# Kernel tuning notes

Measured on AMD Instinct MI355X. Metric: run time of the kernel, lower is better.

The kernel has to match this reference:

```python
import jax, jax.numpy as jnp
import numpy as np

# Cap on neighbors per query. The original op returns ragged (data-dependent
# length) neighbor lists, which is impossible under jit; we return a padded
# [M, K] representation plus row_splits built from the true (capped) counts.
K = 64


def setup_inputs() -> dict:
    key = jax.random.key(0)
    kp, kq = jax.random.split(key)
    points = jax.random.normal(kp, (16384, 3), dtype=jnp.float32)
    queries = jax.random.normal(kq, (8192, 3), dtype=jnp.float32)
    radius = jnp.asarray(0.15, dtype=jnp.float32)
    return {"points": points, "queries": queries, "radius": radius}


def _pairwise_sqdist(queries, points):
    # ||q-p||^2 = ||q||^2 + ||p||^2 - 2 q.p  (avoids an [M,N,3] intermediate)
    q2 = jnp.sum(queries * queries, axis=-1)  # [M]
    p2 = jnp.sum(points * points, axis=-1)    # [N]
    d2 = q2[:, None] + p2[None, :] - 2.0 * (queries @ points.T)  # [M,N]
    return jnp.maximum(d2, 0.0)


def reference(points, queries, radius):
    # metric='L2' -> squared distances, ignore_query_point=False,
    # return_distances=True.
    d2 = _pairwise_sqdist(queries, points)          # [M, N]
    mask = d2 <= radius * radius                    # neighbor membership
    # Select up to K closest in-radius neighbors per query via top_k on -d2.
    neg = jnp.where(mask, -d2, -jnp.inf)
    vals, idx = jax.lax.top_k(neg, K)               # [M, K]
    valid = vals > -jnp.inf                         # which slots hold real neighbors
    counts = jnp.sum(valid.astype(jnp.int64), axis=-1)          # [M]
    neighbors_row_splits = jnp.concatenate(
        [jnp.zeros((1,), jnp.int64), jnp.cumsum(counts)])       # [M+1]
    neighbors_index = jnp.where(valid, idx, -1)                 # [M, K], -1 pad
    neighbors_distance = jnp.where(valid, -vals, 0.0)           # [M, K], squared L2
    return neighbors_index, neighbors_row_splits, neighbors_distance
```

## Files before the change

### kernel.cpp

```cpp
#include <hip/hip_runtime.h>
#include <math.h>

#pragma clang fp contract(off)

#define KCAP 64
#define QPW 4
#define WAVES 4
#define BLOCK (WAVES * 64)
#define QPB (QPW * WAVES)
#define SLABS 4
#define TILE 1024

__global__ __launch_bounds__(256) void prep_kernel(
    const float* __restrict__ pts, float4* __restrict__ soa,
    int* __restrict__ counts, int N, int M) {
  int i = blockIdx.x * 256 + threadIdx.x;
  if (i < N) {
    float x = pts[i * 3 + 0];
    float y = pts[i * 3 + 1];
    float z = pts[i * 3 + 2];
    soa[i] = make_float4(x, y, z, (x * x + y * y) + z * z);
  }
  if (i < M) counts[i] = 0;
}

__global__ __launch_bounds__(BLOCK, 8) void search_kernel(
    const float4* __restrict__ soa, const float* __restrict__ queries,
    const float* __restrict__ radius_p, float* __restrict__ out_idx,
    float* __restrict__ out_dist, int* __restrict__ counts, int N, int M) {
  __shared__ float4 tile[TILE];
  const int tid = threadIdx.x;
  const int lane = tid & 63;
  const int wave = tid >> 6;
  const float r = radius_p[0];
  const float rr = r * r;
  const int qbase = (blockIdx.x * WAVES + wave) * QPW;
  const int slab = N / SLABS;
  const int slab_begin = blockIdx.y * slab;
  const int slab_end = slab_begin + slab;

  float qx[QPW], qy[QPW], qz[QPW], q2[QPW];
#pragma unroll
  for (int g = 0; g < QPW; ++g) {
    int q = qbase + g;
    float x = queries[q * 3 + 0];
    float y = queries[q * 3 + 1];
    float z = queries[q * 3 + 2];
    qx[g] = x; qy[g] = y; qz[g] = z;
    q2[g] = (x * x + y * y) + z * z;
  }

  for (int base = slab_begin; base < slab_end; base += TILE) {
    for (int i = tid; i < TILE; i += BLOCK) tile[i] = soa[base + i];
    __syncthreads();
#pragma unroll 4
    for (int it = 0; it < TILE / 64; ++it) {
      int j = it * 64 + lane;
      float4 p = tile[j];
      float d2v[QPW];
      bool hit[QPW];
      bool any = false;
#pragma unroll
      for (int g = 0; g < QPW; ++g) {
        float dot = fmaf(p.z, qz[g], fmaf(p.y, qy[g], p.x * qx[g]));
        float s = q2[g] + p.w;
        float d2 = fmaf(dot, -2.0f, s);
        d2 = fmaxf(d2, 0.0f);
        d2v[g] = d2;
        hit[g] = (d2 <= rr);
        any = any | hit[g];
      }
      if (any) {
#pragma unroll
        for (int g = 0; g < QPW; ++g)
          if (hit[g]) {
            int q = qbase + g;
            int pos = atomicAdd(&counts[q], 1);
            if (pos < KCAP) {
              out_dist[q * KCAP + pos] = d2v[g];
              out_idx[q * KCAP + pos] = (float)(base + j);
            }
          }
      }
    }
    __syncthreads();
  }
}

__global__ __launch_bounds__(256) void sort_kernel(
    float* __restrict__ out_idx, float* __restrict__ out_dist,
    int* __restrict__ counts, int M) {
  int q = blockIdx.x * (256 / 64) + (threadIdx.x >> 6);
  if (q >= M) return;
  int lane = threadIdx.x & 63;
  int c = counts[q];
  int c64 = c < KCAP ? c : KCAP;
  float d2 = (lane < c64) ? out_dist[q * KCAP + lane] : INFINITY;
  int idx = (lane < c64) ? (int)out_idx[q * KCAP + lane] : 0x7fffffff;
  for (int k = 2; k <= 64; k <<= 1) {
    for (int jj = k >> 1; jj > 0; jj >>= 1) {
      float od2 = __shfl_xor(d2, jj);
      int oidx = __shfl_xor(idx, jj);
      bool up = ((lane & k) == 0);
      bool lower = ((lane & jj) == 0);
      bool takeMin = (lower == up);
      bool oLess = (od2 < d2) || (od2 == d2 && oidx < idx);
      bool take = takeMin ? oLess : !oLess;
      if (take) { d2 = od2; idx = oidx; }
    }
  }
  out_idx[q * KCAP + lane] = (lane < c64) ? (float)idx : -1.0f;
  out_dist[q * KCAP + lane] = (lane < c64) ? d2 : 0.0f;
  if (lane == 0 && c != c64) counts[q] = c64;
}

__global__ __launch_bounds__(1024) void scan_kernel(
    const int* __restrict__ counts, float* __restrict__ rs, int M) {
  __shared__ int part[1024];
  const int tid = threadIdx.x;
  const int base = tid * 8;
  int loc[8];
  int s = 0;
  for (int j = 0; j < 8; ++j) {
    int c = (base + j < M) ? counts[base + j] : 0;
    c = c < KCAP ? c : KCAP;
    s += c;
    loc[j] = s;
  }
  part[tid] = s;
  __syncthreads();
  for (int off = 1; off < 1024; off <<= 1) {
    int v = (tid >= off) ? part[tid - off] : 0;
    __syncthreads();
    part[tid] += v;
    __syncthreads();
  }
  int excl = part[tid] - s;
  if (tid == 0) rs[0] = 0.0f;
  for (int j = 0; j < 8; ++j)
    if (base + j < M) rs[1 + base + j] = (float)(excl + loc[j]);
}

extern "C" void kernel_launch(void* const* d_in, const int* in_sizes, int n_in,
                              void* d_out, int out_size, void* d_ws, size_t ws_size,
                              hipStream_t stream) {
  const float* points = (const float*)d_in[0];
  const float* queries = (const float*)d_in[1];
  const float* radius = (const float*)d_in[2];
  const int N = in_sizes[0] / 3;
  const int M = in_sizes[1] / 3;

  float* out = (float*)d_out;
  float* out_idx = out;
  float* out_rs = out + (size_t)M * KCAP;
  float* out_dist = out_rs + (M + 1);

  float4* soa = (float4*)d_ws;
  int* counts = (int*)(soa + N);

  int prep_n = (N > M ? N : M);
  prep_kernel<<<(prep_n + 255) / 256, 256, 0, stream>>>(points, soa, counts, N, M);

  dim3 grid((M + QPB - 1) / QPB, SLABS);
  search_kernel<<<grid, BLOCK, 0, stream>>>(soa, queries, radius, out_idx,
                                            out_dist, counts, N, M);

  sort_kernel<<<(M + 3) / 4, 256, 0, stream>>>(out_idx, out_dist, counts, M);
  scan_kernel<<<1, 1024, 0, stream>>>(counts, out_rs, M);
}
```

Measured before the change: 52.57 us.

## Fuse prep into search, merge sort and scan, double queries per wave

Removes the prep kernel: the search kernel now loads AoS points directly into the shared tile and computes the squared norm there, and the counts are zeroed with a memset. Queries per wave go from 4 to 8 and slabs from 4 to 8, which gives more point reuse per tile load and more blocks, at the cost of more registers (launch bounds occupancy lowered to 6). The clamp to zero moves off the hot path into the rare hit branch. The sort and scan kernels are merged into a single finalize launch whose last block performs a wave-shuffle scan, cutting one launch.

New measurement: 67.69 us. 28.8% more time.

```diff
diff --git a/kernel.cpp b/kernel.cpp
--- a/kernel.cpp
+++ b/kernel.cpp
@@ -4,28 +4,15 @@
 #pragma clang fp contract(off)
 
 #define KCAP 64
-#define QPW 4
+#define QPW 8
 #define WAVES 4
 #define BLOCK (WAVES * 64)
 #define QPB (QPW * WAVES)
-#define SLABS 4
+#define SLABS 8
 #define TILE 1024
 
-__global__ __launch_bounds__(256) void prep_kernel(
-    const float* __restrict__ pts, float4* __restrict__ soa,
-    int* __restrict__ counts, int N, int M) {
-  int i = blockIdx.x * 256 + threadIdx.x;
-  if (i < N) {
-    float x = pts[i * 3 + 0];
-    float y = pts[i * 3 + 1];
-    float z = pts[i * 3 + 2];
-    soa[i] = make_float4(x, y, z, (x * x + y * y) + z * z);
-  }
-  if (i < M) counts[i] = 0;
-}
-
-__global__ __launch_bounds__(BLOCK, 8) void search_kernel(
-    const float4* __restrict__ soa, const float* __restrict__ queries,
+__global__ __launch_bounds__(BLOCK, 6) void search_kernel(
+    const float* __restrict__ pts, const float* __restrict__ queries,
     const float* __restrict__ radius_p, float* __restrict__ out_idx,
     float* __restrict__ out_dist, int* __restrict__ counts, int N, int M) {
   __shared__ float4 tile[TILE];
@@ -35,25 +22,40 @@
   const float r = radius_p[0];
   const float rr = r * r;
   const int qbase = (blockIdx.x * WAVES + wave) * QPW;
-  const int slab = N / SLABS;
-  const int slab_begin = blockIdx.y * slab;
-  const int slab_end = slab_begin + slab;
+  const int slab = (N + SLABS - 1) / SLABS;
+  const int sb = blockIdx.y * slab;
+  const int se = min(N, sb + slab);
 
   float qx[QPW], qy[QPW], qz[QPW], q2[QPW];
 #pragma unroll
   for (int g = 0; g < QPW; ++g) {
     int q = qbase + g;
-    float x = queries[q * 3 + 0];
-    float y = queries[q * 3 + 1];
-    float z = queries[q * 3 + 2];
-    qx[g] = x; qy[g] = y; qz[g] = z;
-    q2[g] = (x * x + y * y) + z * z;
+    if (q < M) {
+      float x = queries[q * 3 + 0];
+      float y = queries[q * 3 + 1];
+      float z = queries[q * 3 + 2];
+      qx[g] = x; qy[g] = y; qz[g] = z;
+      q2[g] = (x * x + y * y) + z * z;
+    } else {
+      qx[g] = 0.f; qy[g] = 0.f; qz[g] = 0.f;
+      q2[g] = INFINITY;
+    }
   }
 
-  for (int base = slab_begin; base < slab_end; base += TILE) {
-    for (int i = tid; i < TILE; i += BLOCK) tile[i] = soa[base + i];
+  for (int base = sb; base < se; base += TILE) {
+    for (int i = tid; i < TILE; i += BLOCK) {
+      int p = base + i;
+      float x = 0.f, y = 0.f, z = 0.f, p2 = INFINITY;
+      if (p < se) {
+        x = pts[p * 3 + 0];
+        y = pts[p * 3 + 1];
+        z = pts[p * 3 + 2];
+        p2 = (x * x + y * y) + z * z;
+      }
+      tile[i] = make_float4(x, y, z, p2);
+    }
     __syncthreads();
-#pragma unroll 4
+#pragma unroll 2
     for (int it = 0; it < TILE / 64; ++it) {
       int j = it * 64 + lane;
       float4 p = tile[j];
@@ -65,19 +67,18 @@
         float dot = fmaf(p.z, qz[g], fmaf(p.y, qy[g], p.x * qx[g]));
         float s = q2[g] + p.w;
         float d2 = fmaf(dot, -2.0f, s);
-        d2 = fmaxf(d2, 0.0f);
         d2v[g] = d2;
         hit[g] = (d2 <= rr);
         any = any | hit[g];
       }
-      if (any) {
+      if (__builtin_expect(any, 0)) {
 #pragma unroll
         for (int g = 0; g < QPW; ++g)
           if (hit[g]) {
             int q = qbase + g;
             int pos = atomicAdd(&counts[q], 1);
             if (pos < KCAP) {
-              out_dist[q * KCAP + pos] = d2v[g];
+              out_dist[q * KCAP + pos] = fmaxf(d2v[g], 0.0f);
               out_idx[q * KCAP + pos] = (float)(base + j);
             }
           }
@@ -87,58 +88,70 @@
   }
 }
 
-__global__ __launch_bounds__(256) void sort_kernel(
+__global__ __launch_bounds__(256) void finalize_kernel(
     float* __restrict__ out_idx, float* __restrict__ out_dist,
-    int* __restrict__ counts, int M) {
-  int q = blockIdx.x * (256 / 64) + (threadIdx.x >> 6);
-  if (q >= M) return;
-  int lane = threadIdx.x & 63;
-  int c = counts[q];
-  int c64 = c < KCAP ? c : KCAP;
-  float d2 = (lane < c64) ? out_dist[q * KCAP + lane] : INFINITY;
-  int idx = (lane < c64) ? (int)out_idx[q * KCAP + lane] : 0x7fffffff;
-  for (int k = 2; k <= 64; k <<= 1) {
-    for (int jj = k >> 1; jj > 0; jj >>= 1) {
-      float od2 = __shfl_xor(d2, jj);
-      int oidx = __shfl_xor(idx, jj);
-      bool up = ((lane & k) == 0);
-      bool lower = ((lane & jj) == 0);
-      bool takeMin = (lower == up);
-      bool oLess = (od2 < d2) || (od2 == d2 && oidx < idx);
-      bool take = takeMin ? oLess : !oLess;
-      if (take) { d2 = od2; idx = oidx; }
+    const int* __restrict__ counts, float* __restrict__ rs, int M) {
+  const int b = blockIdx.x;
+  const int nsort = gridDim.x - 1;
+  const int tid = threadIdx.x;
+  const int lane = tid & 63;
+  const int wave = tid >> 6;
+
+  if (b < nsort) {
+#pragma unroll 1
+    for (int g = 0; g < QPW; ++g) {
+      int q = (b * WAVES + wave) * QPW + g;
+      if (q >= M) break;
+      int c = counts[q];
+      int c64 = c < KCAP ? c : KCAP;
+      float d2 = (lane < c64) ? out_dist[q * KCAP + lane] : INFINITY;
+      int idx = (lane < c64) ? (int)out_idx[q * KCAP + lane] : 0x7fffffff;
+      for (int k = 2; k <= 64; k <<= 1) {
+        for (int jj = k >> 1; jj > 0; jj >>= 1) {
+          float od2 = __shfl_xor(d2, jj);
+          int oidx = __shfl_xor(idx, jj);
+          bool up = ((lane & k) == 0);
+          bool lower = ((lane & jj) == 0);
+          bool takeMin = (lower == up);
+          bool oLess = (od2 < d2) || (od2 == d2 && oidx < idx);
+          bool take = takeMin ? oLess : !oLess;
+          if (take) { d2 = od2; idx = oidx; }
+        }
+      }
+      out_idx[q * KCAP + lane] = (lane < c64) ? (float)idx : -1.0f;
+      out_dist[q * KCAP + lane] = (lane < c64) ? d2 : 0.0f;
+    }
+  } else {
+    __shared__ int wsum[WAVES];
+    const int base = tid * 32;
+    int s = 0;
+#pragma unroll 4
+    for (int j = 0; j < 32; ++j) {
+      int i = base + j;
+      int c = (i < M) ? counts[i] : 0;
+      s += (c < KCAP ? c : KCAP);
+    }
+    int pre = s;
+    for (int off = 1; off < 64; off <<= 1) {
+      int v = __shfl_up(pre, off);
+      if (lane >= off) pre += v;
+    }
+    if (lane == 63) wsum[wave] = pre;
+    __syncthreads();
+    int woff = 0;
+    for (int w = 0; w < wave; ++w) woff += wsum[w];
+    int run = woff + pre - s;
+    if (tid == 0) rs[0] = 0.0f;
+#pragma unroll 4
+    for (int j = 0; j < 32; ++j) {
+      int i = base + j;
+      if (i < M) {
+        int c = counts[i];
+        run += (c < KCAP ? c : KCAP);
+        rs[1 + i] = (float)run;
+      }
     }
   }
-  out_idx[q * KCAP + lane] = (lane < c64) ? (float)idx : -1.0f;
-  out_dist[q * KCAP + lane] = (lane < c64) ? d2 : 0.0f;
-  if (lane == 0 && c != c64) counts[q] = c64;
-}
-
-__global__ __launch_bounds__(1024) void scan_kernel(
-    const int* __restrict__ counts, float* __restrict__ rs, int M) {
-  __shared__ int part[1024];
-  const int tid = threadIdx.x;
-  const int base = tid * 8;
-  int loc[8];
-  int s = 0;
-  for (int j = 0; j < 8; ++j) {
-    int c = (base + j < M) ? counts[base + j] : 0;
-    c = c < KCAP ? c : KCAP;
-    s += c;
-    loc[j] = s;
-  }
-  part[tid] = s;
-  __syncthreads();
-  for (int off = 1; off < 1024; off <<= 1) {
-    int v = (tid >= off) ? part[tid - off] : 0;
-    __syncthreads();
-    part[tid] += v;
-    __syncthreads();
-  }
-  int excl = part[tid] - s;
-  if (tid == 0) rs[0] = 0.0f;
-  for (int j = 0; j < 8; ++j)
-    if (base + j < M) rs[1 + base + j] = (float)(excl + loc[j]);
 }
 
 extern "C" void kernel_launch(void* const* d_in, const int* in_sizes, int n_in,
@@ -154,17 +167,15 @@
   float* out_idx = out;
   float* out_rs = out + (size_t)M * KCAP;
   float* out_dist = out_rs + (M + 1);
+  int* counts = (int*)d_ws;
 
-  float4* soa = (float4*)d_ws;
-  int* counts = (int*)(soa + N);
-
-  int prep_n = (N > M ? N : M);
-  prep_kernel<<<(prep_n + 255) / 256, 256, 0, stream>>>(points, soa, counts, N, M);
+  hipMemsetAsync(counts, 0, (size_t)M * sizeof(int), stream);
 
   dim3 grid((M + QPB - 1) / QPB, SLABS);
-  search_kernel<<<grid, BLOCK, 0, stream>>>(soa, queries, radius, out_idx,
+  search_kernel<<<grid, BLOCK, 0, stream>>>(points, queries, radius, out_idx,
                                             out_dist, counts, N, M);
 
-  sort_kernel<<<(M + 3) / 4, 256, 0, stream>>>(out_idx, out_dist, counts, M);
-  scan_kernel<<<1, 1024, 0, stream>>>(counts, out_rs, M);
+  const int nsort = (M + QPB - 1) / QPB;
+  finalize_kernel<<<nsort + 1, 256, 0, stream>>>(out_idx, out_dist, counts,
+                                                 out_rs, M);
 }
```
